# Kernel optimization log

Hardware: AMD Instinct MI355X
Metric: run time of the kernel (lower is better)

## Reference

```python
import jax, jax.numpy as jnp
import numpy as np

N_NODES = 100000
N_EDGES = 1600000
IN_DIM = 128
OUT_DIM = 128


def setup_inputs() -> dict:
    key = jax.random.key(0)
    ks = jax.random.split(key, 8)
    x = jax.random.normal(ks[0], (N_NODES, IN_DIM), dtype=jnp.float32)
    one_hot_h = jax.random.normal(ks[1], (N_NODES, OUT_DIM), dtype=jnp.float32)
    # three candidate-op linear transforms (in_dim -> out_dim)
    W0 = jax.random.normal(ks[2], (IN_DIM, OUT_DIM), dtype=jnp.float32) * 0.05
    W1 = jax.random.normal(ks[3], (IN_DIM, OUT_DIM), dtype=jnp.float32) * 0.05
    W2 = jax.random.normal(ks[4], (IN_DIM, OUT_DIM), dtype=jnp.float32) * 0.05
    # sparse mask_matrix in COO form: out[r] += v * H[c]
    mask_rows = jax.random.randint(ks[5], (N_EDGES,), 0, N_NODES, dtype=jnp.int32)
    mask_cols = jax.random.randint(ks[6], (N_EDGES,), 0, N_NODES, dtype=jnp.int32)
    mask_vals = jax.random.uniform(ks[7], (N_EDGES,), dtype=jnp.float32)
    return {"x": x, "one_hot_h": one_hot_h, "W0": W0, "W1": W1, "W2": W2,
            "mask_rows": mask_rows, "mask_cols": mask_cols, "mask_vals": mask_vals}


def reference(x, one_hot_h, W0, W1, W2, mask_rows, mask_cols, mask_vals):
    # Original: sum_k spmm(mask_matrix, op_k(x)) + spmm(mask_matrix, one_hot_h).
    # spmm is linear, so summing per-op outputs pre-aggregation is exact and
    # fuses K spmm launches into one sparse aggregation pass.
    H = x @ W0 + x @ W1 + x @ W2 + one_hot_h              # [N, out_dim]
    gathered = mask_vals[:, None] * H[mask_cols]          # [E, out_dim]
    out = jax.ops.segment_sum(gathered, mask_rows, num_segments=x.shape[0])
    return out
```

## Files before the change

kernel.cpp:

```cpp
#include <hip/hip_runtime.h>
#include <hip/hip_bf16.h>

#define N_NODES 100000
#define N_EDGES 1600000
#define DIM 128

#define NBIN 256
#define RPP  391
#define PCAP 8192
#define P1_BLOCKS 256
#define CHUNK (N_EDGES / P1_BLOCKS)

typedef unsigned int uint_t;
typedef unsigned short ushort_t;
typedef float f32x4 __attribute__((ext_vector_type(4)));
typedef __bf16 bf16x8 __attribute__((ext_vector_type(8)));

__device__ inline ushort_t f2bf(float f) {
    uint_t u = __float_as_uint(f);
    uint_t r = (u + 0x7FFFu + ((u >> 16) & 1u)) >> 16;
    return (ushort_t)r;
}
__device__ inline float bf2f(uint_t lo16) { return __uint_as_float(lo16 << 16); }

__global__ __launch_bounds__(256) void pass1_bin(
        const int* __restrict__ rows, const int* __restrict__ cols,
        const float* __restrict__ vals, int* __restrict__ psize,
        long long* __restrict__ slab,
        const float* __restrict__ W0, const float* __restrict__ W1,
        const float* __restrict__ W2, ushort_t* __restrict__ WT) {
    if (blockIdx.x >= P1_BLOCKS) {
        int i = (blockIdx.x - P1_BLOCKS) * 256 + threadIdx.x;
        if (i < DIM * DIM) {
            int m = i & 127, k = i >> 7;
            float s = W0[k * DIM + m] + W1[k * DIM + m] + W2[k * DIM + m];
            WT[m * DIM + k] = f2bf(s);
        }
        return;
    }
    __shared__ int hist[NBIN];
    __shared__ int binoff[NBIN];
    __shared__ int resv[NBIN];
    __shared__ int curs[NBIN];
    __shared__ long long ebuf[CHUNK];
    __shared__ int edest[CHUNK];

    int t = threadIdx.x;
    int e0 = blockIdx.x * CHUNK;

    if (t < NBIN) hist[t] = 0;
    __syncthreads();

    for (int i = t; i < CHUNK; i += 256) {
        int r = rows[e0 + i];
        atomicAdd(&hist[r / RPP], 1);
    }
    __syncthreads();

    if (t < 64) {
        int b = t * 4;
        int v0 = hist[b], v1 = hist[b + 1], v2 = hist[b + 2], v3 = hist[b + 3];
        int s = v0 + v1 + v2 + v3;
        int incl = s;
#pragma unroll
        for (int d = 1; d < 64; d <<= 1) {
            int o = __shfl_up(incl, d, 64);
            if (t >= d) incl += o;
        }
        int excl = incl - s;
        binoff[b]     = excl;
        binoff[b + 1] = excl + v0;
        binoff[b + 2] = excl + v0 + v1;
        binoff[b + 3] = excl + v0 + v1 + v2;
    }
    __syncthreads();

    if (t < NBIN) {
        int len = hist[t];
        int r = (len > 0) ? atomicAdd(&psize[t], len) : 0;
        resv[t] = t * PCAP + r;
        curs[t] = binoff[t];
    }
    __syncthreads();

    for (int i = t; i < CHUNK; i += 256) {
        int   r = rows[e0 + i];
        int   c = cols[e0 + i];
        float v = vals[e0 + i];
        int b  = r / RPP;
        int lr = r - b * RPP;
        int pos = atomicAdd(&curs[b], 1);
        uint_t key = ((uint_t)lr << 17) | (uint_t)c;
        ebuf[pos]  = ((long long)__float_as_int(v) << 32) | (long long)key;
        edest[pos] = resv[b] + (pos - binoff[b]);
    }
    __syncthreads();

    for (int i = t; i < CHUNK; i += 256)
        slab[edest[i]] = ebuf[i];
}

__global__ void pscan(const int* __restrict__ psize, int* __restrict__ pbase,
                      int* __restrict__ off) {
    int lane = threadIdx.x & 63;
    int b = lane * 4;
    int v0 = min(psize[b], PCAP),     v1 = min(psize[b + 1], PCAP);
    int v2 = min(psize[b + 2], PCAP), v3 = min(psize[b + 3], PCAP);
    int s = v0 + v1 + v2 + v3;
    int incl = s;
#pragma unroll
    for (int d = 1; d < 64; d <<= 1) {
        int o = __shfl_up(incl, d, 64);
        if (lane >= d) incl += o;
    }
    int excl = incl - s;
    pbase[b]     = excl;
    pbase[b + 1] = excl + v0;
    pbase[b + 2] = excl + v0 + v1;
    pbase[b + 3] = excl + v0 + v1 + v2;
    if (lane == 0) off[N_NODES] = N_EDGES;
}

__global__ __launch_bounds__(256) void pass2_sort(
        const long long* __restrict__ slab, const int* __restrict__ psize,
        const int* __restrict__ pbase, int* __restrict__ off,
        long long* __restrict__ csr) {
    __shared__ int cnt[RPP + 1];
    __shared__ int loff[RPP + 1];
    __shared__ int curs[RPP];
    __shared__ long long ebuf[PCAP];

    int p = blockIdx.x, t = threadIdx.x;
    int n = min(psize[p], PCAP);
    int base = pbase[p];
    int rlo = p * RPP;
    int nrows = N_NODES - rlo; if (nrows > RPP) nrows = RPP;
    const long long* seg = slab + (long long)p * PCAP;

    for (int i = t; i < RPP + 1; i += 256) cnt[i] = 0;
    __syncthreads();

    for (int i = t; i < n; i += 256) {
        uint_t key = (uint_t)(seg[i] & 0xFFFFFFFFll);
        atomicAdd(&cnt[key >> 17], 1);
    }
    __syncthreads();

    if (t < 64) {
        int b7 = t * 7;
        int v[7]; int s = 0;
#pragma unroll
        for (int k = 0; k < 7; ++k) {
            int idx = b7 + k;
            v[k] = (idx < RPP) ? cnt[idx] : 0;
            s += v[k];
        }
        int incl = s;
#pragma unroll
        for (int d = 1; d < 64; d <<= 1) {
            int o = __shfl_up(incl, d, 64);
            if (t >= d) incl += o;
        }
        int run = incl - s;
#pragma unroll
        for (int k = 0; k < 7; ++k) {
            int idx = b7 + k;
            if (idx < RPP) loff[idx] = run;
            run += v[k];
        }
    }
    __syncthreads();

    for (int i = t; i < nrows; i += 256) {
        curs[i] = loff[i];
        off[rlo + i] = base + loff[i];
    }
    __syncthreads();

    for (int i = t; i < n; i += 256) {
        long long ev = seg[i];
        uint_t key = (uint_t)(ev & 0xFFFFFFFFll);
        int lr = key >> 17;
        uint_t c = key & 0x1FFFFu;
        int pos = atomicAdd(&curs[lr], 1);
        ebuf[pos] = (long long)(((unsigned long long)ev & 0xFFFFFFFF00000000ull) | c);
    }
    __syncthreads();

    for (int i = t; i < n; i += 256)
        __builtin_nontemporal_store(ebuf[i], &csr[base + i]);
}

__global__ __launch_bounds__(256) void gemm_mfma(const float* __restrict__ x,
                                                 const float* __restrict__ oh,
                                                 const ushort_t* __restrict__ WT,
                                                 uint_t* __restrict__ H16) {
    int tid = threadIdx.x;
    int wv = tid >> 6, l = tid & 63;
    int lr = l & 15, kg = l >> 4;
    int hr = blockIdx.x * 64 + wv * 16 + lr;
    int hr_c = (hr < N_NODES) ? hr : (N_NODES - 1);

    f32x4 acc[8] = {};
    const float* xrow = x + (size_t)hr_c * DIM;

#pragma unroll
    for (int s = 0; s < 4; ++s) {
        float4 xa = *(const float4*)(xrow + s * 32 + kg * 8);
        float4 xb = *(const float4*)(xrow + s * 32 + kg * 8 + 4);
        union { bf16x8 v; __bf16 h[8]; } b;
        b.h[0] = (__bf16)xa.x; b.h[1] = (__bf16)xa.y;
        b.h[2] = (__bf16)xa.z; b.h[3] = (__bf16)xa.w;
        b.h[4] = (__bf16)xb.x; b.h[5] = (__bf16)xb.y;
        b.h[6] = (__bf16)xb.z; b.h[7] = (__bf16)xb.w;
#pragma unroll
        for (int mt = 0; mt < 8; ++mt) {
            bf16x8 a = *(const bf16x8*)&WT[(mt * 16 + lr) * DIM + s * 32 + kg * 8];
            acc[mt] = __builtin_amdgcn_mfma_f32_16x16x32_bf16(a, b.v, acc[mt], 0, 0, 0);
        }
    }

    if (hr < N_NODES) {
#pragma unroll
        for (int mt = 0; mt < 8; ++mt) {
            int c0 = mt * 16 + kg * 4;
            float4 o = *(const float4*)&oh[(size_t)hr * DIM + c0];
            float f0 = acc[mt].x + o.x, f1 = acc[mt].y + o.y;
            float f2 = acc[mt].z + o.z, f3 = acc[mt].w + o.w;
            uint2 pk;
            pk.x = (uint_t)f2bf(f0) | ((uint_t)f2bf(f1) << 16);
            pk.y = (uint_t)f2bf(f2) | ((uint_t)f2bf(f3) << 16);
            *(uint2*)&H16[(size_t)hr * (DIM / 2) + c0 / 2] = pk;
        }
    }
}

__global__ __launch_bounds__(256) void gather_kernel(const uint_t* __restrict__ H16,
                                                     const int* __restrict__ off,
                                                     const long long* __restrict__ csr,
                                                     float* __restrict__ out) {
    int tid  = threadIdx.x;
    int wave = tid >> 6;
    int lane = tid & 63;
    int grp  = lane >> 4;
    int il   = lane & 15;
    int wid  = blockIdx.x * 16 + wave * 4 + grp;

    int s = off[wid], e = off[wid + 1];
    float acc[8] = {0.f, 0.f, 0.f, 0.f, 0.f, 0.f, 0.f, 0.f};

    int p = s;
    for (; p + 3 < e; p += 4) {
        long long cv0 = __builtin_nontemporal_load(&csr[p]);
        long long cv1 = __builtin_nontemporal_load(&csr[p + 1]);
        long long cv2 = __builtin_nontemporal_load(&csr[p + 2]);
        long long cv3 = __builtin_nontemporal_load(&csr[p + 3]);
        uint4 h0 = *(const uint4*)&H16[(long long)(int)(cv0 & 0x1FFFF) * (DIM / 2) + il * 4];
        uint4 h1 = *(const uint4*)&H16[(long long)(int)(cv1 & 0x1FFFF) * (DIM / 2) + il * 4];
        uint4 h2 = *(const uint4*)&H16[(long long)(int)(cv2 & 0x1FFFF) * (DIM / 2) + il * 4];
        uint4 h3 = *(const uint4*)&H16[(long long)(int)(cv3 & 0x1FFFF) * (DIM / 2) + il * 4];
        float v0 = __int_as_float((int)(cv0 >> 32));
        float v1 = __int_as_float((int)(cv1 >> 32));
        float v2 = __int_as_float((int)(cv2 >> 32));
        float v3 = __int_as_float((int)(cv3 >> 32));
#define ACC8(h, v)                                                        \
        acc[0] += (v) * bf2f((h).x & 0xFFFFu); acc[1] += (v) * bf2f((h).x >> 16); \
        acc[2] += (v) * bf2f((h).y & 0xFFFFu); acc[3] += (v) * bf2f((h).y >> 16); \
        acc[4] += (v) * bf2f((h).z & 0xFFFFu); acc[5] += (v) * bf2f((h).z >> 16); \
        acc[6] += (v) * bf2f((h).w & 0xFFFFu); acc[7] += (v) * bf2f((h).w >> 16);
        ACC8(h0, v0) ACC8(h1, v1) ACC8(h2, v2) ACC8(h3, v3)
    }
    for (; p < e; ++p) {
        long long cv = __builtin_nontemporal_load(&csr[p]);
        float v = __int_as_float((int)(cv >> 32));
        uint4 h = *(const uint4*)&H16[(long long)(int)(cv & 0x1FFFF) * (DIM / 2) + il * 4];
        ACC8(h, v)
    }
#undef ACC8

    float* op = &out[(long long)wid * DIM + il * 8];
    f32x4 o0 = {acc[0], acc[1], acc[2], acc[3]};
    f32x4 o1 = {acc[4], acc[5], acc[6], acc[7]};
    __builtin_nontemporal_store(o0, (f32x4*)op);
    __builtin_nontemporal_store(o1, (f32x4*)(op + 4));
}

extern "C" void kernel_launch(void* const* d_in, const int* in_sizes, int n_in,
                              void* d_out, int out_size, void* d_ws, size_t ws_size,
                              hipStream_t stream) {
    const float* x    = (const float*)d_in[0];
    const float* oh   = (const float*)d_in[1];
    const float* W0   = (const float*)d_in[2];
    const float* W1   = (const float*)d_in[3];
    const float* W2   = (const float*)d_in[4];
    const int*   rows = (const int*)d_in[5];
    const int*   cols = (const int*)d_in[6];
    const float* vals = (const float*)d_in[7];
    float* out = (float*)d_out;

    char* p = (char*)d_ws;
    size_t oW    = 0;
    size_t oH    = oW + 64 * 1024;
    size_t oOff  = oH + (size_t)N_NODES * DIM * 2;
    size_t oPs   = oOff + (size_t)(N_NODES + 32) * 4;
    size_t oPb   = oPs + 2048;
    size_t oSlab = oPb + 2048;
    size_t oCsr  = oSlab + (size_t)NBIN * PCAP * 8;

    ushort_t*  WT    = (ushort_t*)(p + oW);
    uint_t*    H16   = (uint_t*)(p + oH);
    int*       off   = (int*)(p + oOff);
    int*       psize = (int*)(p + oPs);
    int*       pbase = (int*)(p + oPb);
    long long* slab  = (long long*)(p + oSlab);
    long long* csr   = (long long*)(p + oCsr);

    (void)hipMemsetAsync(psize, 0, NBIN * sizeof(int), stream);
    pass1_bin<<<P1_BLOCKS + 64, 256, 0, stream>>>(rows, cols, vals, psize, slab,
                                                  W0, W1, W2, WT);
    pscan<<<1, 64, 0, stream>>>(psize, pbase, off);
    gemm_mfma<<<(N_NODES + 63) / 64, 256, 0, stream>>>(x, oh, WT, H16);
    pass2_sort<<<NBIN, 256, 0, stream>>>(slab, psize, pbase, off, csr);
    gather_kernel<<<N_NODES / 16, 256, 0, stream>>>(H16, off, csr, out);
}
```

Baseline: 164.9 us.

## Fold partition scan into sort kernel, deepen gather unroll, stream GEMM inputs

Removes the standalone single-block pscan launch by having every pass2_sort block recompute the 256-entry prefix scan into shared memory, and reorders the launches so the sort runs before the GEMM. The gather kernel now unrolls by 8 with two independent accumulator sets, issuing more outstanding H loads per edge group and shortening FMA dependency chains. The GEMM reads x and one_hot_h with nontemporal loads to avoid polluting cache. Each sort block does a small redundant scan, and the extra registers in the gather loop could lower occupancy.

```diff
diff --git a/kernel.cpp b/kernel.cpp
--- a/kernel.cpp
+++ b/kernel.cpp
@@ -100,45 +100,45 @@
         slab[edest[i]] = ebuf[i];
 }
 
-__global__ void pscan(const int* __restrict__ psize, int* __restrict__ pbase,
-                      int* __restrict__ off) {
-    int lane = threadIdx.x & 63;
-    int b = lane * 4;
-    int v0 = min(psize[b], PCAP),     v1 = min(psize[b + 1], PCAP);
-    int v2 = min(psize[b + 2], PCAP), v3 = min(psize[b + 3], PCAP);
-    int s = v0 + v1 + v2 + v3;
-    int incl = s;
-#pragma unroll
-    for (int d = 1; d < 64; d <<= 1) {
-        int o = __shfl_up(incl, d, 64);
-        if (lane >= d) incl += o;
-    }
-    int excl = incl - s;
-    pbase[b]     = excl;
-    pbase[b + 1] = excl + v0;
-    pbase[b + 2] = excl + v0 + v1;
-    pbase[b + 3] = excl + v0 + v1 + v2;
-    if (lane == 0) off[N_NODES] = N_EDGES;
-}
-
 __global__ __launch_bounds__(256) void pass2_sort(
         const long long* __restrict__ slab, const int* __restrict__ psize,
-        const int* __restrict__ pbase, int* __restrict__ off,
-        long long* __restrict__ csr) {
+        int* __restrict__ off, long long* __restrict__ csr) {
+    __shared__ int pb[NBIN + 1];
     __shared__ int cnt[RPP + 1];
     __shared__ int loff[RPP + 1];
     __shared__ int curs[RPP];
     __shared__ long long ebuf[PCAP];
 
     int p = blockIdx.x, t = threadIdx.x;
+
+    if (t < 64) {
+        int b = t * 4;
+        int v0 = min(psize[b], PCAP),     v1 = min(psize[b + 1], PCAP);
+        int v2 = min(psize[b + 2], PCAP), v3 = min(psize[b + 3], PCAP);
+        int s = v0 + v1 + v2 + v3;
+        int incl = s;
+#pragma unroll
+        for (int d = 1; d < 64; d <<= 1) {
+            int o = __shfl_up(incl, d, 64);
+            if (t >= d) incl += o;
+        }
+        int excl = incl - s;
+        pb[b]     = excl;
+        pb[b + 1] = excl + v0;
+        pb[b + 2] = excl + v0 + v1;
+        pb[b + 3] = excl + v0 + v1 + v2;
+        if (t == 63) pb[NBIN] = incl;
+    }
+    for (int i = t; i < RPP + 1; i += 256) cnt[i] = 0;
+    __syncthreads();
+
     int n = min(psize[p], PCAP);
-    int base = pbase[p];
+    int base = pb[p];
     int rlo = p * RPP;
     int nrows = N_NODES - rlo; if (nrows > RPP) nrows = RPP;
     const long long* seg = slab + (long long)p * PCAP;
 
-    for (int i = t; i < RPP + 1; i += 256) cnt[i] = 0;
-    __syncthreads();
+    if (p == NBIN - 1 && t == 0) off[N_NODES] = pb[NBIN];
 
     for (int i = t; i < n; i += 256) {
         uint_t key = (uint_t)(seg[i] & 0xFFFFFFFFll);
@@ -206,8 +206,8 @@
 
 #pragma unroll
     for (int s = 0; s < 4; ++s) {
-        float4 xa = *(const float4*)(xrow + s * 32 + kg * 8);
-        float4 xb = *(const float4*)(xrow + s * 32 + kg * 8 + 4);
+        f32x4 xa = __builtin_nontemporal_load((const f32x4*)(xrow + s * 32 + kg * 8));
+        f32x4 xb = __builtin_nontemporal_load((const f32x4*)(xrow + s * 32 + kg * 8 + 4));
         union { bf16x8 v; __bf16 h[8]; } b;
         b.h[0] = (__bf16)xa.x; b.h[1] = (__bf16)xa.y;
         b.h[2] = (__bf16)xa.z; b.h[3] = (__bf16)xa.w;
@@ -224,7 +224,7 @@
 #pragma unroll
         for (int mt = 0; mt < 8; ++mt) {
             int c0 = mt * 16 + kg * 4;
-            float4 o = *(const float4*)&oh[(size_t)hr * DIM + c0];
+            f32x4 o = __builtin_nontemporal_load((const f32x4*)&oh[(size_t)hr * DIM + c0]);
             float f0 = acc[mt].x + o.x, f1 = acc[mt].y + o.y;
             float f2 = acc[mt].z + o.z, f3 = acc[mt].w + o.w;
             uint2 pk;
@@ -247,40 +247,60 @@
     int wid  = blockIdx.x * 16 + wave * 4 + grp;
 
     int s = off[wid], e = off[wid + 1];
-    float acc[8] = {0.f, 0.f, 0.f, 0.f, 0.f, 0.f, 0.f, 0.f};
+    float acc0[8] = {}, acc1[8] = {};
+
+#define ACC8(A, h, v)                                                      \
+        A[0] += (v) * bf2f((h).x & 0xFFFFu); A[1] += (v) * bf2f((h).x >> 16); \
+        A[2] += (v) * bf2f((h).y & 0xFFFFu); A[3] += (v) * bf2f((h).y >> 16); \
+        A[4] += (v) * bf2f((h).z & 0xFFFFu); A[5] += (v) * bf2f((h).z >> 16); \
+        A[6] += (v) * bf2f((h).w & 0xFFFFu); A[7] += (v) * bf2f((h).w >> 16);
 
     int p = s;
+    for (; p + 7 < e; p += 8) {
+        long long cv[8];
+#pragma unroll
+        for (int k = 0; k < 8; ++k)
+            cv[k] = __builtin_nontemporal_load(&csr[p + k]);
+        uint4 h[8];
+#pragma unroll
+        for (int k = 0; k < 8; ++k)
+            h[k] = *(const uint4*)&H16[(long long)(int)(cv[k] & 0x1FFFF) * (DIM / 2) + il * 4];
+#pragma unroll
+        for (int k = 0; k < 8; k += 2) {
+            float va = __int_as_float((int)(cv[k] >> 32));
+            float vb = __int_as_float((int)(cv[k + 1] >> 32));
+            ACC8(acc0, h[k], va)
+            ACC8(acc1, h[k + 1], vb)
+        }
+    }
     for (; p + 3 < e; p += 4) {
-        long long cv0 = __builtin_nontemporal_load(&csr[p]);
-        long long cv1 = __builtin_nontemporal_load(&csr[p + 1]);
-        long long cv2 = __builtin_nontemporal_load(&csr[p + 2]);
-        long long cv3 = __builtin_nontemporal_load(&csr[p + 3]);
-        uint4 h0 = *(const uint4*)&H16[(long long)(int)(cv0 & 0x1FFFF) * (DIM / 2) + il * 4];
-        uint4 h1 = *(const uint4*)&H16[(long long)(int)(cv1 & 0x1FFFF) * (DIM / 2) + il * 4];
-        uint4 h2 = *(const uint4*)&H16[(long long)(int)(cv2 & 0x1FFFF) * (DIM / 2) + il * 4];
-        uint4 h3 = *(const uint4*)&H16[(long long)(int)(cv3 & 0x1FFFF) * (DIM / 2) + il * 4];
-        float v0 = __int_as_float((int)(cv0 >> 32));
-        float v1 = __int_as_float((int)(cv1 >> 32));
-        float v2 = __int_as_float((int)(cv2 >> 32));
-        float v3 = __int_as_float((int)(cv3 >> 32));
-#define ACC8(h, v)                                                        \
-        acc[0] += (v) * bf2f((h).x & 0xFFFFu); acc[1] += (v) * bf2f((h).x >> 16); \
-        acc[2] += (v) * bf2f((h).y & 0xFFFFu); acc[3] += (v) * bf2f((h).y >> 16); \
-        acc[4] += (v) * bf2f((h).z & 0xFFFFu); acc[5] += (v) * bf2f((h).z >> 16); \
-        acc[6] += (v) * bf2f((h).w & 0xFFFFu); acc[7] += (v) * bf2f((h).w >> 16);
-        ACC8(h0, v0) ACC8(h1, v1) ACC8(h2, v2) ACC8(h3, v3)
+        long long cv[4];
+#pragma unroll
+        for (int k = 0; k < 4; ++k)
+            cv[k] = __builtin_nontemporal_load(&csr[p + k]);
+        uint4 h[4];
+#pragma unroll
+        for (int k = 0; k < 4; ++k)
+            h[k] = *(const uint4*)&H16[(long long)(int)(cv[k] & 0x1FFFF) * (DIM / 2) + il * 4];
+#pragma unroll
+        for (int k = 0; k < 4; k += 2) {
+            float va = __int_as_float((int)(cv[k] >> 32));
+            float vb = __int_as_float((int)(cv[k + 1] >> 32));
+            ACC8(acc0, h[k], va)
+            ACC8(acc1, h[k + 1], vb)
+        }
     }
     for (; p < e; ++p) {
         long long cv = __builtin_nontemporal_load(&csr[p]);
         float v = __int_as_float((int)(cv >> 32));
         uint4 h = *(const uint4*)&H16[(long long)(int)(cv & 0x1FFFF) * (DIM / 2) + il * 4];
-        ACC8(h, v)
+        ACC8(acc0, h, v)
     }
 #undef ACC8
 
     float* op = &out[(long long)wid * DIM + il * 8];
-    f32x4 o0 = {acc[0], acc[1], acc[2], acc[3]};
-    f32x4 o1 = {acc[4], acc[5], acc[6], acc[7]};
+    f32x4 o0 = {acc0[0] + acc1[0], acc0[1] + acc1[1], acc0[2] + acc1[2], acc0[3] + acc1[3]};
+    f32x4 o1 = {acc0[4] + acc1[4], acc0[5] + acc1[5], acc0[6] + acc1[6], acc0[7] + acc1[7]};
     __builtin_nontemporal_store(o0, (f32x4*)op);
     __builtin_nontemporal_store(o1, (f32x4*)(op + 4));
 }
@@ -303,23 +323,20 @@
     size_t oH    = oW + 64 * 1024;
     size_t oOff  = oH + (size_t)N_NODES * DIM * 2;
     size_t oPs   = oOff + (size_t)(N_NODES + 32) * 4;
-    size_t oPb   = oPs + 2048;
-    size_t oSlab = oPb + 2048;
+    size_t oSlab = oPs + 4096;
     size_t oCsr  = oSlab + (size_t)NBIN * PCAP * 8;
 
     ushort_t*  WT    = (ushort_t*)(p + oW);
     uint_t*    H16   = (uint_t*)(p + oH);
     int*       off   = (int*)(p + oOff);
     int*       psize = (int*)(p + oPs);
-    int*       pbase = (int*)(p + oPb);
     long long* slab  = (long long*)(p + oSlab);
     long long* csr   = (long long*)(p + oCsr);
 
     (void)hipMemsetAsync(psize, 0, NBIN * sizeof(int), stream);
     pass1_bin<<<P1_BLOCKS + 64, 256, 0, stream>>>(rows, cols, vals, psize, slab,
                                                   W0, W1, W2, WT);
-    pscan<<<1, 64, 0, stream>>>(psize, pbase, off);
+    pass2_sort<<<NBIN, 256, 0, stream>>>(slab, psize, off, csr);
     gemm_mfma<<<(N_NODES + 63) / 64, 256, 0, stream>>>(x, oh, WT, H16);
-    pass2_sort<<<NBIN, 256, 0, stream>>>(slab, psize, pbase, off, csr);
     gather_kernel<<<N_NODES / 16, 256, 0, stream>>>(H16, off, csr, out);
 }
```

Result: slower. 169.7 us (+2.9%).
